# Optimization experiments

Hardware: AMD Instinct MI355X
Metric: run time of the kernel (lower is better)

## Reference

```python
import jax, jax.numpy as jnp
import numpy as np

D_MODEL = 1024
D_FF = 4096
N_EXPERTS = 8
TOP_K = 2

def setup_inputs() -> dict:
    key = jax.random.key(0)
    ks = jax.random.split(key, 8)
    s = 0.02
    return {
        "x": jax.random.normal(ks[0], (4, 2048, D_MODEL), dtype=jnp.float32),
        "W1": jax.random.normal(ks[1], (N_EXPERTS, D_MODEL, D_FF), dtype=jnp.float32) * s,
        "b1": jnp.zeros((N_EXPERTS, D_FF), dtype=jnp.float32),
        "W2": jax.random.normal(ks[2], (N_EXPERTS, D_FF, D_MODEL), dtype=jnp.float32) * s,
        "b2": jnp.zeros((N_EXPERTS, D_MODEL), dtype=jnp.float32),
        "Wg": jax.random.normal(ks[3], (D_MODEL, N_EXPERTS), dtype=jnp.float32) * s,
        "bg": jnp.zeros((N_EXPERTS,), dtype=jnp.float32),
    }

def reference(x, W1, b1, W2, b2, Wg, bg):
    B, S, D = x.shape
    # Gating network
    gate_logits = jnp.einsum('bsd,de->bse', x, Wg) + bg
    gate_probs = jax.nn.softmax(gate_logits, axis=-1)  # (B,S,E)
    # Top-k routing on softmax probs (matches torch.topk(F.softmax(logits)))
    top_k_probs, top_k_indices = jax.lax.top_k(gate_probs, TOP_K)  # (B,S,k)
    T = B * S
    x_flat = x.reshape(T, D)
    idx_flat = top_k_indices.reshape(T, TOP_K)
    prob_flat = top_k_probs.reshape(T, TOP_K)
    # Per-token combine weight for each expert: sum of top-k probs routed to it
    # combine[t, e] = sum_j prob_flat[t, j] * (idx_flat[t, j] == e)
    onehot = jax.nn.one_hot(idx_flat, N_EXPERTS, dtype=x.dtype)  # (T,k,E)
    combine = jnp.einsum('tk,tke->te', prob_flat, onehot)  # (T,E)
    out = jnp.zeros((T, D), dtype=x.dtype)
    for e in range(N_EXPERTS):  # static small loop over experts
        h = jax.nn.relu(x_flat @ W1[e] + b1[e])  # (T, d_ff)
        y = h @ W2[e] + b2[e]                    # (T, d_model)
        out = out + combine[:, e:e+1] * y
    return out.reshape(B, S, D), gate_probs
```

## Files before the change

kernel.cpp:

```cpp
#include <hip/hip_runtime.h>

#define D_MODEL 1024
#define D_FF    4096
#define N_EXP   8
#define BM 128
#define BN 128
#define BK 64

typedef __attribute__((ext_vector_type(8))) short bf16x8;
typedef __attribute__((ext_vector_type(4))) float f32x4;
typedef unsigned int u32;

__device__ __forceinline__ unsigned short f2bf(float f) {
  union { float f; unsigned u; } v; v.f = f;
  unsigned r = v.u + 0x7FFFu + ((v.u >> 16) & 1u);
  return (unsigned short)(r >> 16);
}

__device__ __forceinline__ void gl_lds16(const void* g, void* l) {
  __builtin_amdgcn_global_load_lds((const __attribute__((address_space(1))) u32*)g,
                                   (__attribute__((address_space(3))) u32*)l, 16, 0, 0);
}

__global__ void convert_x_kernel(const float* __restrict__ x,
                                 unsigned short* __restrict__ xb, int total8) {
  int i = blockIdx.x * blockDim.x + threadIdx.x;
  if (i >= total8) return;
  const float4* src = (const float4*)x + (size_t)i * 2;
  float4 a = src[0], b = src[1];
  ushort4 lo, hi;
  lo.x = f2bf(a.x); lo.y = f2bf(a.y); lo.z = f2bf(a.z); lo.w = f2bf(a.w);
  hi.x = f2bf(b.x); hi.y = f2bf(b.y); hi.z = f2bf(b.z); hi.w = f2bf(b.w);
  ushort4* dst = (ushort4*)xb + (size_t)i * 2;
  dst[0] = lo; dst[1] = hi;
}

__global__ __launch_bounds__(256)
void transpose_convert_kernel(const float* __restrict__ src, unsigned short* __restrict__ dst,
                              int Ksub, int Nsrc, int k0, int n0, int Nchunk,
                              unsigned long long eStride) {
  __shared__ u32 s32k[32][65];
  int e = blockIdx.z;
  int kb = blockIdx.x * 64, nb = blockIdx.y * 64;
  const float* se = src + (size_t)e * eStride + (size_t)(k0 + kb) * Nsrc + (n0 + nb);
  unsigned short* de = dst + (size_t)e * Nchunk * Ksub + (size_t)nb * Ksub + kb;
  int tid = threadIdx.x;
  int kh = tid >> 4;
  int n4 = (tid & 15) * 4;
  #pragma unroll
  for (int p = 0; p < 2; p++) {
    int k = kh * 2 + p * 32;
    float4 v0 = *(const float4*)(se + (size_t)k * Nsrc + n4);
    float4 v1 = *(const float4*)(se + (size_t)(k + 1) * Nsrc + n4);
    #pragma unroll
    for (int j = 0; j < 4; j++) {
      u32 pk = (u32)f2bf(((const float*)&v0)[j]) |
               ((u32)f2bf(((const float*)&v1)[j]) << 16);
      s32k[k >> 1][n4 + j] = pk;
    }
  }
  __syncthreads();
  #pragma unroll
  for (int c = 0; c < 2; c++) {
    int id = tid + c * 256;
    int n = id >> 3, kc = id & 7;
    uint4 o;
    o.x = s32k[kc * 4 + 0][n];
    o.y = s32k[kc * 4 + 1][n];
    o.z = s32k[kc * 4 + 2][n];
    o.w = s32k[kc * 4 + 3][n];
    *(uint4*)(de + (size_t)n * Ksub + kc * 8) = o;
  }
}

__global__ void gating_kernel(const float* __restrict__ x,
                              const float* __restrict__ Wg,
                              const float* __restrict__ bg,
                              float* __restrict__ gate_out,
                              int* __restrict__ cnt,
                              int* __restrict__ tokIdx,
                              float* __restrict__ tokW, int T) {
  int wv = threadIdx.x >> 6, lane = threadIdx.x & 63;
  int t = blockIdx.x * 4 + wv;
  if (t >= T) return;
  const float* xr = x + (size_t)t * D_MODEL + lane * 16;
  float acc[N_EXP];
  #pragma unroll
  for (int e = 0; e < N_EXP; e++) acc[e] = 0.f;
  #pragma unroll
  for (int q = 0; q < 4; q++) {
    float4 xv = *(const float4*)(xr + q * 4);
    #pragma unroll
    for (int r = 0; r < 4; r++) {
      float xs = ((const float*)&xv)[r];
      const float* wrow = Wg + (size_t)(lane * 16 + q * 4 + r) * N_EXP;
      float4 wa = *(const float4*)wrow;
      float4 wb = *(const float4*)(wrow + 4);
      acc[0] += xs * wa.x; acc[1] += xs * wa.y; acc[2] += xs * wa.z; acc[3] += xs * wa.w;
      acc[4] += xs * wb.x; acc[5] += xs * wb.y; acc[6] += xs * wb.z; acc[7] += xs * wb.w;
    }
  }
  #pragma unroll
  for (int off = 32; off > 0; off >>= 1) {
    #pragma unroll
    for (int e = 0; e < N_EXP; e++) acc[e] += __shfl_xor(acc[e], off);
  }
  if (lane == 0) {
    float l[N_EXP], p[N_EXP];
    float m = -1e30f;
    #pragma unroll
    for (int e = 0; e < N_EXP; e++) { l[e] = acc[e] + bg[e]; m = fmaxf(m, l[e]); }
    float s = 0.f;
    #pragma unroll
    for (int e = 0; e < N_EXP; e++) { p[e] = __expf(l[e] - m); s += p[e]; }
    float inv = 1.f / s;
    #pragma unroll
    for (int e = 0; e < N_EXP; e++) { p[e] *= inv; gate_out[(size_t)t * N_EXP + e] = p[e]; }
    int e1 = 0;
    #pragma unroll
    for (int e = 1; e < N_EXP; e++) if (p[e] > p[e1]) e1 = e;
    int e2 = (e1 == 0) ? 1 : 0;
    #pragma unroll
    for (int e = 0; e < N_EXP; e++) if (e != e1 && p[e] > p[e2]) e2 = e;
    int pos = atomicAdd(cnt + e1, 1);
    tokIdx[(size_t)e1 * T + pos] = t; tokW[(size_t)e1 * T + pos] = p[e1];
    pos = atomicAdd(cnt + e2, 1);
    tokIdx[(size_t)e2 * T + pos] = t; tokW[(size_t)e2 * T + pos] = p[e2];
  }
}

__global__ void schedule_kernel(const int* __restrict__ cnt, int* __restrict__ meta,
                                int* __restrict__ tE, int* __restrict__ tB,
                                int* __restrict__ tV, int T, int maxTiles) {
  if (threadIdx.x != 0 || blockIdx.x != 0) return;
  int t = 0;
  for (int e = 0; e < N_EXP; e++) {
    int c = cnt[e];
    for (int r = 0; r < c && t < maxTiles; r += BM) {
      tE[t] = e; tB[t] = e * T + r; tV[t] = min(BM, c - r); t++;
    }
  }
  meta[0] = t;
}

__global__ __launch_bounds__(256)
void gemm1_kernel(const unsigned short* __restrict__ xb,
                  const unsigned short* __restrict__ w1t,
                  const float* __restrict__ b1,
                  const int* __restrict__ meta,
                  const int* __restrict__ tE, const int* __restrict__ tB,
                  const int* __restrict__ tV, const int* __restrict__ tokIdx,
                  unsigned short* __restrict__ h, int FFC, int chunk_off, int ncolLog2) {
  __shared__ unsigned short As[BM * BK];
  __shared__ unsigned short Bs[BN * BK];
  __shared__ int stok[BM];

  int total = gridDim.x;
  int L = blockIdx.x;
  int q = total >> 3, r8 = total & 7;
  int xcd = L & 7, idx = L >> 3;
  int work = (xcd < r8) ? (xcd * (q + 1) + idx) : (r8 * (q + 1) + (xcd - r8) * q + idx);
  int ncol = 1 << ncolLog2;
  int tile = work >> ncolLog2;
  int cb = work & (ncol - 1);
  if (tile >= meta[0]) return;
  int e = tE[tile], base = tB[tile], valid = tV[tile];
  int tid = threadIdx.x;

  if (tid < BM) stok[tid] = tokIdx[base + (tid < valid ? tid : valid - 1)];
  __syncthreads();

  int w = tid >> 6, lane = tid & 63;
  int lr = lane >> 3, lc = lane & 7;

  const unsigned short* panel = w1t + (size_t)e * FFC * D_MODEL;
  const unsigned short* aBase[4];
  const unsigned short* bBase[4];
  #pragma unroll
  for (int p = 0; p < 4; p++) {
    int row = (w * 4 + p) * 8 + lr;
    int cA = (lc - row) & 7;
    aBase[p] = xb + (size_t)stok[row] * D_MODEL + cA * 8;
    int cB = (lc - row) & 7;
    bBase[p] = panel + (size_t)(cb * BN + row) * D_MODEL + cB * 8;
  }

  int wr = w >> 1, wc = w & 1;
  int l15 = lane & 15, l4 = lane >> 4;
  int aOff[2][4], bOff[2][4];
  #pragma unroll
  for (int kk = 0; kk < 2; kk++) {
    #pragma unroll
    for (int m = 0; m < 4; m++) {
      int row = wr * 64 + m * 16 + l15;
      int c = kk * 4 + l4;
      aOff[kk][m] = row * 64 + (((c + row) & 7) << 3);
      int col = wc * 64 + m * 16 + l15;
      bOff[kk][m] = col * 64 + (((c + col) & 7) << 3);
    }
  }

  f32x4 acc[4][4];
  #pragma unroll
  for (int m = 0; m < 4; m++)
    #pragma unroll
    for (int n = 0; n < 4; n++) acc[m][n] = (f32x4){0.f, 0.f, 0.f, 0.f};

  for (int kt = 0; kt < D_MODEL / BK; kt++) {
    #pragma unroll
    for (int p = 0; p < 4; p++)
      gl_lds16(aBase[p] + kt * BK, &As[(w * 4 + p) * 512]);
    #pragma unroll
    for (int p = 0; p < 4; p++)
      gl_lds16(bBase[p] + kt * BK, &Bs[(w * 4 + p) * 512]);
    __syncthreads();
    #pragma unroll
    for (int kk = 0; kk < 2; kk++) {
      bf16x8 a[4], b[4];
      #pragma unroll
      for (int m = 0; m < 4; m++) a[m] = *(const bf16x8*)&As[aOff[kk][m]];
      #pragma unroll
      for (int n = 0; n < 4; n++) b[n] = *(const bf16x8*)&Bs[bOff[kk][n]];
      #pragma unroll
      for (int m = 0; m < 4; m++)
        #pragma unroll
        for (int n = 0; n < 4; n++)
          acc[m][n] = __builtin_amdgcn_mfma_f32_16x16x32_bf16(a[m], b[n], acc[m][n], 0, 0, 0);
    }
    __syncthreads();
  }

  #pragma unroll
  for (int n = 0; n < 4; n++) {
    int colc = cb * BN + wc * 64 + n * 16 + l15;
    float bias = b1[(size_t)e * D_FF + chunk_off + colc];
    #pragma unroll
    for (int m = 0; m < 4; m++) {
      #pragma unroll
      for (int r = 0; r < 4; r++) {
        int row = wr * 64 + m * 16 + l4 * 4 + r;
        float v = acc[m][n][r] + bias;
        v = v > 0.f ? v : 0.f;
        h[(size_t)(tile * BM + row) * FFC + colc] = f2bf(v);
      }
    }
  }
}

__global__ __launch_bounds__(256)
void gemm2_kernel(const unsigned short* __restrict__ h,
                  const unsigned short* __restrict__ w2t,
                  const float* __restrict__ b2,
                  const int* __restrict__ meta,
                  const int* __restrict__ tE, const int* __restrict__ tB,
                  const int* __restrict__ tV, const int* __restrict__ tokIdx,
                  const float* __restrict__ tokW,
                  float* __restrict__ out, int FFC, int chunk_off) {
  __shared__ unsigned short As[BM * BK];
  __shared__ unsigned short Bs[BN * BK];
  __shared__ int stok[BM];
  __shared__ float sw[BM];

  int total = gridDim.x;
  int L = blockIdx.x;
  int q = total >> 3, r8 = total & 7;
  int xcd = L & 7, idx = L >> 3;
  int work = (xcd < r8) ? (xcd * (q + 1) + idx) : (r8 * (q + 1) + (xcd - r8) * q + idx);
  int tile = work >> 3;
  int cb = work & 7;
  if (tile >= meta[0]) return;
  int e = tE[tile], base = tB[tile], valid = tV[tile];
  int tid = threadIdx.x;

  if (tid < BM) {
    int rr = tid < valid ? tid : valid - 1;
    stok[tid] = tokIdx[base + rr];
    sw[tid] = tokW[base + rr];
  }
  __syncthreads();

  int w = tid >> 6, lane = tid & 63;
  int lr = lane >> 3, lc = lane & 7;

  const unsigned short* panel = w2t + (size_t)e * D_MODEL * FFC;
  const unsigned short* aBase[4];
  const unsigned short* bBase[4];
  #pragma unroll
  for (int p = 0; p < 4; p++) {
    int row = (w * 4 + p) * 8 + lr;
    int cA = (lc - row) & 7;
    aBase[p] = h + (size_t)(tile * BM + row) * FFC + cA * 8;
    int cB = (lc - row) & 7;
    bBase[p] = panel + (size_t)(cb * BN + row) * FFC + cB * 8;
  }

  int wr = w >> 1, wc = w & 1;
  int l15 = lane & 15, l4 = lane >> 4;
  int aOff[2][4], bOff[2][4];
  #pragma unroll
  for (int kk = 0; kk < 2; kk++) {
    #pragma unroll
    for (int m = 0; m < 4; m++) {
      int row = wr * 64 + m * 16 + l15;
      int c = kk * 4 + l4;
      aOff[kk][m] = row * 64 + (((c + row) & 7) << 3);
      int col = wc * 64 + m * 16 + l15;
      bOff[kk][m] = col * 64 + (((c + col) & 7) << 3);
    }
  }

  f32x4 acc[4][4];
  #pragma unroll
  for (int m = 0; m < 4; m++)
    #pragma unroll
    for (int n = 0; n < 4; n++) acc[m][n] = (f32x4){0.f, 0.f, 0.f, 0.f};

  int KT = FFC / BK;
  for (int kt = 0; kt < KT; kt++) {
    #pragma unroll
    for (int p = 0; p < 4; p++)
      gl_lds16(aBase[p] + kt * BK, &As[(w * 4 + p) * 512]);
    #pragma unroll
    for (int p = 0; p < 4; p++)
      gl_lds16(bBase[p] + kt * BK, &Bs[(w * 4 + p) * 512]);
    __syncthreads();
    #pragma unroll
    for (int kk = 0; kk < 2; kk++) {
      bf16x8 a[4], b[4];
      #pragma unroll
      for (int m = 0; m < 4; m++) a[m] = *(const bf16x8*)&As[aOff[kk][m]];
      #pragma unroll
      for (int n = 0; n < 4; n++) b[n] = *(const bf16x8*)&Bs[bOff[kk][n]];
      #pragma unroll
      for (int m = 0; m < 4; m++)
        #pragma unroll
        for (int n = 0; n < 4; n++)
          acc[m][n] = __builtin_amdgcn_mfma_f32_16x16x32_bf16(a[m], b[n], acc[m][n], 0, 0, 0);
    }
    __syncthreads();
  }

  int addBias = (chunk_off == 0) ? 1 : 0;
  #pragma unroll
  for (int n = 0; n < 4; n++) {
    int colg = cb * BN + wc * 64 + n * 16 + l15;
    float bias = addBias ? b2[(size_t)e * D_MODEL + colg] : 0.f;
    #pragma unroll
    for (int m = 0; m < 4; m++) {
      #pragma unroll
      for (int r = 0; r < 4; r++) {
        int row = wr * 64 + m * 16 + l4 * 4 + r;
        if (row < valid) {
          float v = (acc[m][n][r] + bias) * sw[row];
          atomicAdd(out + (size_t)stok[row] * D_MODEL + colg, v);
        }
      }
    }
  }
}

extern "C" void kernel_launch(void* const* d_in, const int* in_sizes, int n_in,
                              void* d_out, int out_size, void* d_ws, size_t ws_size,
                              hipStream_t stream) {
  const float* x  = (const float*)d_in[0];
  const float* W1 = (const float*)d_in[1];
  const float* b1 = (const float*)d_in[2];
  const float* W2 = (const float*)d_in[3];
  const float* b2 = (const float*)d_in[4];
  const float* Wg = (const float*)d_in[5];
  const float* bg = (const float*)d_in[6];

  int T = in_sizes[0] / D_MODEL;
  float* out = (float*)d_out;
  float* gate_out = out + (size_t)T * D_MODEL;

  char* ws = (char*)d_ws;
  int* cnt  = (int*)(ws + 0);
  int* meta = (int*)(ws + 64);
  int* tE   = (int*)(ws + 128);
  int* tB   = (int*)(ws + 1024);
  int* tV   = (int*)(ws + 2048);
  size_t off = 4096;
  int* tokIdx = (int*)(ws + off);   off += (size_t)N_EXP * T * 4;
  float* tokW = (float*)(ws + off); off += (size_t)N_EXP * T * 4;
  unsigned short* xb = (unsigned short*)(ws + off); off += (size_t)T * D_MODEL * 2;
  off = (off + 255) & ~(size_t)255;

  int maxTiles = (2 * T) / BM + N_EXP;
  int FFC = D_FF;
  while (FFC > 256 &&
         off + (size_t)FFC * (16384 + 16384 + (size_t)maxTiles * BM * 2) > ws_size)
    FFC >>= 1;

  unsigned short* w1t = (unsigned short*)(ws + off); off += (size_t)FFC * 16384;
  unsigned short* w2t = (unsigned short*)(ws + off); off += (size_t)FFC * 16384;
  unsigned short* h   = (unsigned short*)(ws + off);

  hipMemsetAsync(d_out, 0, (size_t)T * D_MODEL * sizeof(float), stream);
  hipMemsetAsync(cnt, 0, N_EXP * sizeof(int), stream);

  int total8 = T * D_MODEL / 8;
  convert_x_kernel<<<(total8 + 255) / 256, 256, 0, stream>>>(x, xb, total8);
  gating_kernel<<<(T + 3) / 4, 256, 0, stream>>>(x, Wg, bg, gate_out, cnt, tokIdx, tokW, T);
  schedule_kernel<<<1, 64, 0, stream>>>(cnt, meta, tE, tB, tV, T, maxTiles);

  int ncol1 = FFC / BN;
  int ncol1Log2 = __builtin_ctz(ncol1);
  for (int c = 0; c * FFC < D_FF; c++) {
    transpose_convert_kernel<<<dim3(D_MODEL / 64, FFC / 64, N_EXP), 256, 0, stream>>>(
        W1, w1t, D_MODEL, D_FF, 0, c * FFC, FFC, (unsigned long long)D_MODEL * D_FF);
    transpose_convert_kernel<<<dim3(FFC / 64, D_MODEL / 64, N_EXP), 256, 0, stream>>>(
        W2, w2t, FFC, D_MODEL, c * FFC, 0, D_MODEL, (unsigned long long)D_FF * D_MODEL);
    gemm1_kernel<<<maxTiles * ncol1, 256, 0, stream>>>(
        xb, w1t, b1, meta, tE, tB, tV, tokIdx, h, FFC, c * FFC, ncol1Log2);
    gemm2_kernel<<<maxTiles * (D_MODEL / BN), 256, 0, stream>>>(
        h, w2t, b2, meta, tE, tB, tV, tokIdx, tokW, out, FFC, c * FFC);
  }
}
```

Before: 795.7 us.

## Fuse x bf16 conversion into gating and split-K gemm2 across two blocks

```diff
diff --git a/kernel.cpp b/kernel.cpp
--- a/kernel.cpp
+++ b/kernel.cpp
@@ -20,19 +20,6 @@
 __device__ __forceinline__ void gl_lds16(const void* g, void* l) {
   __builtin_amdgcn_global_load_lds((const __attribute__((address_space(1))) u32*)g,
                                    (__attribute__((address_space(3))) u32*)l, 16, 0, 0);
-}
-
-__global__ void convert_x_kernel(const float* __restrict__ x,
-                                 unsigned short* __restrict__ xb, int total8) {
-  int i = blockIdx.x * blockDim.x + threadIdx.x;
-  if (i >= total8) return;
-  const float4* src = (const float4*)x + (size_t)i * 2;
-  float4 a = src[0], b = src[1];
-  ushort4 lo, hi;
-  lo.x = f2bf(a.x); lo.y = f2bf(a.y); lo.z = f2bf(a.z); lo.w = f2bf(a.w);
-  hi.x = f2bf(b.x); hi.y = f2bf(b.y); hi.z = f2bf(b.z); hi.w = f2bf(b.w);
-  ushort4* dst = (ushort4*)xb + (size_t)i * 2;
-  dst[0] = lo; dst[1] = hi;
 }
 
 __global__ __launch_bounds__(256)
@@ -77,6 +64,7 @@
                               const float* __restrict__ Wg,
                               const float* __restrict__ bg,
                               float* __restrict__ gate_out,
+                              unsigned short* __restrict__ xb,
                               int* __restrict__ cnt,
                               int* __restrict__ tokIdx,
                               float* __restrict__ tokW, int T) {
@@ -87,9 +75,12 @@
   float acc[N_EXP];
   #pragma unroll
   for (int e = 0; e < N_EXP; e++) acc[e] = 0.f;
+  ushort4 xc[4];
   #pragma unroll
   for (int q = 0; q < 4; q++) {
     float4 xv = *(const float4*)(xr + q * 4);
+    xc[q].x = f2bf(xv.x); xc[q].y = f2bf(xv.y);
+    xc[q].z = f2bf(xv.z); xc[q].w = f2bf(xv.w);
     #pragma unroll
     for (int r = 0; r < 4; r++) {
       float xs = ((const float*)&xv)[r];
@@ -100,6 +91,9 @@
       acc[4] += xs * wb.x; acc[5] += xs * wb.y; acc[6] += xs * wb.z; acc[7] += xs * wb.w;
     }
   }
+  unsigned short* xbr = xb + (size_t)t * D_MODEL + lane * 16;
+  #pragma unroll
+  for (int q = 0; q < 4; q++) *(ushort4*)(xbr + q * 4) = xc[q];
   #pragma unroll
   for (int off = 32; off > 0; off >>= 1) {
     #pragma unroll
@@ -266,8 +260,9 @@
   int q = total >> 3, r8 = total & 7;
   int xcd = L & 7, idx = L >> 3;
   int work = (xcd < r8) ? (xcd * (q + 1) + idx) : (r8 * (q + 1) + (xcd - r8) * q + idx);
-  int tile = work >> 3;
-  int cb = work & 7;
+  int tile = work >> 4;
+  int cb = (work >> 1) & 7;
+  int ks = work & 1;
   if (tile >= meta[0]) return;
   int e = tE[tile], base = tB[tile], valid = tV[tile];
   int tid = threadIdx.x;
@@ -282,6 +277,9 @@
   int w = tid >> 6, lane = tid & 63;
   int lr = lane >> 3, lc = lane & 7;
 
+  const int KT = FFC / BK / 2;
+  const int ksOff = ks * KT * BK;
+
   const unsigned short* panel = w2t + (size_t)e * D_MODEL * FFC;
   const unsigned short* aBase[4];
   const unsigned short* bBase[4];
@@ -289,9 +287,9 @@
   for (int p = 0; p < 4; p++) {
     int row = (w * 4 + p) * 8 + lr;
     int cA = (lc - row) & 7;
-    aBase[p] = h + (size_t)(tile * BM + row) * FFC + cA * 8;
+    aBase[p] = h + (size_t)(tile * BM + row) * FFC + ksOff + cA * 8;
     int cB = (lc - row) & 7;
-    bBase[p] = panel + (size_t)(cb * BN + row) * FFC + cB * 8;
+    bBase[p] = panel + (size_t)(cb * BN + row) * FFC + ksOff + cB * 8;
   }
 
   int wr = w >> 1, wc = w & 1;
@@ -315,7 +313,6 @@
     #pragma unroll
     for (int n = 0; n < 4; n++) acc[m][n] = (f32x4){0.f, 0.f, 0.f, 0.f};
 
-  int KT = FFC / BK;
   for (int kt = 0; kt < KT; kt++) {
     #pragma unroll
     for (int p = 0; p < 4; p++)
@@ -340,7 +337,7 @@
     __syncthreads();
   }
 
-  int addBias = (chunk_off == 0) ? 1 : 0;
+  int addBias = (chunk_off == 0 && ks == 0) ? 1 : 0;
   #pragma unroll
   for (int n = 0; n < 4; n++) {
     int colg = cb * BN + wc * 64 + n * 16 + l15;
@@ -399,9 +396,7 @@
   hipMemsetAsync(d_out, 0, (size_t)T * D_MODEL * sizeof(float), stream);
   hipMemsetAsync(cnt, 0, N_EXP * sizeof(int), stream);
 
-  int total8 = T * D_MODEL / 8;
-  convert_x_kernel<<<(total8 + 255) / 256, 256, 0, stream>>>(x, xb, total8);
-  gating_kernel<<<(T + 3) / 4, 256, 0, stream>>>(x, Wg, bg, gate_out, cnt, tokIdx, tokW, T);
+  gating_kernel<<<(T + 3) / 4, 256, 0, stream>>>(x, Wg, bg, gate_out, xb, cnt, tokIdx, tokW, T);
   schedule_kernel<<<1, 64, 0, stream>>>(cnt, meta, tE, tB, tV, T, maxTiles);
 
   int ncol1 = FFC / BN;
@@ -413,7 +408,7 @@
         W2, w2t, FFC, D_MODEL, c * FFC, 0, D_MODEL, (unsigned long long)D_FF * D_MODEL);
     gemm1_kernel<<<maxTiles * ncol1, 256, 0, stream>>>(
         xb, w1t, b1, meta, tE, tB, tV, tokIdx, h, FFC, c * FFC, ncol1Log2);
-    gemm2_kernel<<<maxTiles * (D_MODEL / BN), 256, 0, stream>>>(
+    gemm2_kernel<<<maxTiles * (D_MODEL / BN) * 2, 256, 0, stream>>>(
         h, w2t, b2, meta, tE, tB, tV, tokIdx, tokW, out, FFC, c * FFC);
   }
 }
```

Result: no change. 791.9 us (-0.5%).
